# Kernel optimization log

Measured on AMD Instinct MI355X. Metric: run time of the kernel, lower is better.

Reference implementation:

```python
import jax, jax.numpy as jnp
import numpy as np

PATCH = 9
RAD = PATCH // 2  # 4


def _spatial_correlation(a, b):
    """SpatialCorrelationSampler(kernel_size=1, patch_size=9, stride=1,
    padding=0, dilation_patch=1).
    a, b: [B, C, H, W] -> out: [B, 9, 9, H, W]
    out[b, pi, pj, i, j] = sum_c a[b,c,i,j] * b_zeropad[b,c, i+pi-4, j+pj-4]
    Computed one shift at a time (81 small reductions) so we never
    materialize an 81x-unfolded copy of b.
    """
    B, C, H, W = a.shape
    bp = jnp.pad(b, ((0, 0), (0, 0), (RAD, RAD), (RAD, RAD)))
    rows = []
    for di in range(PATCH):
        cols = []
        for dj in range(PATCH):
            # shifted view of b, then channel-dot with a -> [B, H, W]
            cols.append(jnp.sum(a * bp[:, :, di:di + H, dj:dj + W], axis=1))
        rows.append(jnp.stack(cols, axis=1))  # [B, 9, H, W]
    return jnp.stack(rows, axis=1)  # [B, 9, 9, H, W]


def setup_inputs() -> dict:
    key = jax.random.key(0)
    shapes = [(8, 64, 112, 112), (8, 128, 56, 56), (8, 256, 28, 28), (8, 512, 14, 14)]
    keys = jax.random.split(key, 8)
    inp = {}
    for i, s in enumerate(shapes):
        inp[f"rgb{i}"] = jax.random.normal(keys[i], s, dtype=jnp.float32)
        inp[f"depth{i}"] = jax.random.normal(keys[4 + i], s, dtype=jnp.float32)
    return inp


def reference(rgb0, rgb1, rgb2, rgb3, depth0, depth1, depth2, depth3):
    rgbs = [rgb0, rgb1, rgb2, rgb3]
    depths = [depth0, depth1, depth2, depth3]
    corrs = []
    for i in range(4):
        corrs.insert(0, _spatial_correlation(rgbs[i], depths[i]))
    # reversed order: (corr3, corr2, corr1, corr0)
    return tuple(corrs)
```

## Files before the change

kernel.cpp:

```cpp
#include <hip/hip_runtime.h>
#include <hip/hip_bf16.h>

#define THREADS 256

#define OFF3 0
#define OFF2 127008
#define OFF1 635040
#define OFF0 2667168

#define N1 2032128
#define N2 508032
#define N3 127008
#define WS_L1 0
#define WS_L2 (2 * N1)
#define WS_L3 (WS_L2 + 4 * N2)
#define WS_FLOATS (WS_L3 + 16 * N3)
#define WS_BYTES ((size_t)WS_FLOATS * 4)

#define GB_L0 448
#define GB_L1 224
#define GB_L2 224
#define GB_L3 112
#define GB_TOT (GB_L0 + GB_L1 + GB_L2 + GB_L3)

#define SMEM_FLOATS 9728

typedef __attribute__((ext_vector_type(8))) short bf16x8;
typedef __attribute__((ext_vector_type(4))) float f32x4;

__device__ __attribute__((aligned(64))) const float g_zeropage[16] = {};

__global__ void __launch_bounds__(THREADS)
zero_region_kernel(float* __restrict__ p, int n) {
    int i = blockIdx.x * blockDim.x + threadIdx.x;
    int stride = gridDim.x * blockDim.x;
    for (; i < n; i += stride) p[i] = 0.f;
}

__device__ __forceinline__ void gload16(const float* g, float* l) {
    __builtin_amdgcn_global_load_lds(
        (const __attribute__((address_space(1))) void*)g,
        (__attribute__((address_space(3))) void*)l, 16, 0, 0);
}
__device__ __forceinline__ void gload4(const float* g, float* l) {
    __builtin_amdgcn_global_load_lds(
        (const __attribute__((address_space(1))) void*)g,
        (__attribute__((address_space(3))) void*)l, 4, 0, 0);
}

__device__ __forceinline__ short bf16s(float f) {
    __hip_bfloat16 h = __float2bfloat16(f);
    return *reinterpret_cast<short*>(&h);
}

template<int N> __device__ __forceinline__ void wait_vm_lgkm0() {
    static_assert(N >= 0 && N <= 8, "unsupported count");
    if constexpr (N == 0) asm volatile("s_waitcnt vmcnt(0) lgkmcnt(0)" ::: "memory");
    else if constexpr (N == 1) asm volatile("s_waitcnt vmcnt(1) lgkmcnt(0)" ::: "memory");
    else if constexpr (N == 2) asm volatile("s_waitcnt vmcnt(2) lgkmcnt(0)" ::: "memory");
    else if constexpr (N == 3) asm volatile("s_waitcnt vmcnt(3) lgkmcnt(0)" ::: "memory");
    else if constexpr (N == 4) asm volatile("s_waitcnt vmcnt(4) lgkmcnt(0)" ::: "memory");
    else if constexpr (N == 5) asm volatile("s_waitcnt vmcnt(5) lgkmcnt(0)" ::: "memory");
    else if constexpr (N == 6) asm volatile("s_waitcnt vmcnt(6) lgkmcnt(0)" ::: "memory");
    else if constexpr (N == 7) asm volatile("s_waitcnt vmcnt(7) lgkmcnt(0)" ::: "memory");
    else                       asm volatile("s_waitcnt vmcnt(8) lgkmcnt(0)" ::: "memory");
}

template<int C, int H, int W, int TI, int TW, int SJ, int STRIPS, int CHUNKS,
         int CB, int MODE>
__device__ __forceinline__ void corr_level(const float* __restrict__ a,
                                           const float* __restrict__ b,
                                           float* __restrict__ out,
                                           int blk, float* __restrict__ smem)
{
    constexpr int PER_I = 9 * STRIPS;
    constexpr int USED  = TI * PER_I;
    constexpr bool F4   = (W % 4 == 0) && (TW % 4 == 0) && (SJ % 4 == 0);
    constexpr int BWQ0  = (TW + 8 + 3) / 4 + 1;
    constexpr int BWQ   = (BWQ0 % 2 == 0) ? BWQ0 + 1 : BWQ0;
    constexpr int BW_   = F4 ? BWQ * 4 : (((TW + 8 + 1) / 2) * 2);
    constexpr bool F2   = !F4 && (SJ % 2 == 0) && (TW % 2 == 0);
    constexpr int BROWS = TI + 8;
    constexpr int CCH   = C / CHUNKS;
    constexpr int HT    = (H + TI - 1) / TI;
    constexpr int WT    = W / TW;
    constexpr int NOUT  = 8 * 81 * H * W;
    constexpr int HW    = H * W;
    constexpr int BPC   = BROWS * BW_;
    constexpr int APC   = TI * TW;
    constexpr int NG    = CCH / CB;

    constexpr int F4PR = BW_ / 4;
    constexpr int NBF4 = BROWS * F4PR;
    constexpr int TOT4 = CB * NBF4;
    constexpr int K4   = (TOT4 + THREADS - 1) / THREADS;
    constexpr int TOTS = CB * BPC;
    constexpr int KS   = (TOTS + THREADS - 1) / THREADS;
    constexpr int A4PR = TW / 4;
    constexpr int NAF4 = TI * A4PR;
    constexpr int ATOT4 = CB * NAF4;
    constexpr int KA4  = (ATOT4 + THREADS - 1) / THREADS;
    constexpr int ATOTS = CB * APC;
    constexpr int KAS  = (ATOTS + THREADS - 1) / THREADS;

    constexpr int A_OFF = F4 ? (K4 * THREADS * 4) : (KS * THREADS);
    constexpr int BUFSZ = F4 ? ((K4 + KA4) * THREADS * 4) : ((KS + KAS) * THREADS);
    constexpr int KTOT  = F4 ? (K4 + KA4) : (KS + KAS);

    static_assert(USED <= THREADS && SJ * STRIPS == TW && CCH % CB == 0, "geom");
    static_assert(NG >= 2 && 3 * BUFSZ <= SMEM_FLOATS, "pipeline/smem");

    const int ch = blk % CHUNKS;
    int t = blk / CHUNKS;
    const int jt = t % WT; t /= WT;
    const int it = t % HT;
    const int bb = t / HT;
    const int i0 = it * TI;
    const int jb = jt * TW;

    const int tid = threadIdx.x;
    const int ii  = tid / PER_I;
    const int rem = tid - ii * PER_I;
    const int pi  = rem / STRIPS;
    const int s   = rem - pi * STRIPS;
    const int j0  = s * SJ;
    const bool active = (tid < USED) && ((H % TI == 0) || (i0 + ii) < H);

    const int c0 = ch * CCH;
    const float* __restrict__ bp = b + (size_t)(bb * C + c0) * HW;
    const float* __restrict__ ap = a + (size_t)(bb * C + c0) * HW;
    const float* zp = g_zeropage;

    float acc[9][SJ];
    #pragma unroll
    for (int p = 0; p < 9; ++p)
        #pragma unroll
        for (int u = 0; u < SJ; ++u) acc[p][u] = 0.f;

    const int wbase = tid & ~63;

    auto stage = [&](int cg, float* buf) {
        const float* gb = bp + (size_t)(cg * CB) * HW;
        const float* ga = ap + (size_t)(cg * CB) * HW;
        if constexpr (F4) {
            #pragma unroll
            for (int k = 0; k < K4; ++k) {
                const int f = tid + k * THREADS;
                const int cb  = f / NBF4;
                const int f2  = f - cb * NBF4;
                const int row = f2 / F4PR;
                const int c4  = f2 - row * F4PR;
                const int r   = i0 + row - 4;
                const int jj  = jb + (c4 - 1) * 4;
                const bool ok = (f < TOT4) && ((unsigned)r < (unsigned)H)
                                && (jj >= 0) && (jj <= W - 4);
                const float* src = ok ? (gb + cb * HW + r * W + jj) : zp;
                gload16(src, buf + (size_t)(k * THREADS + wbase) * 4);
            }
            #pragma unroll
            for (int k = 0; k < KA4; ++k) {
                const int f = tid + k * THREADS;
                const int cb  = f / NAF4;
                const int f2  = f - cb * NAF4;
                const int row = f2 / A4PR;
                const int c4  = f2 - row * A4PR;
                const bool ok = (f < ATOT4) && ((H % TI == 0) || (i0 + row) < H);
                const float* src = ok ? (ga + cb * HW + (i0 + row) * W + jb + c4 * 4)
                                      : zp;
                gload16(src, buf + A_OFF + (size_t)(k * THREADS + wbase) * 4);
            }
        } else {
            #pragma unroll
            for (int k = 0; k < KS; ++k) {
                const int f = tid + k * THREADS;
                const int cb  = f / BPC;
                const int f2  = f - cb * BPC;
                const int row = f2 / BW_;
                const int col = f2 - row * BW_;
                const int r   = i0 + row - 4;
                const int jj  = jb + col - 4;
                const bool ok = (f < TOTS) && ((unsigned)r < (unsigned)H)
                                && ((unsigned)jj < (unsigned)W);
                const float* src = ok ? (gb + cb * HW + r * W + jj) : zp;
                gload4(src, buf + (k * THREADS + wbase));
            }
            #pragma unroll
            for (int k = 0; k < KAS; ++k) {
                const int f = tid + k * THREADS;
                const int cb  = f / APC;
                const int f2  = f - cb * APC;
                const int row = f2 / TW;
                const int col = f2 - row * TW;
                const bool ok = (f < ATOTS) && ((H % TI == 0) || (i0 + row) < H);
                const float* src = ok ? (ga + cb * HW + (i0 + row) * W + jb + col)
                                      : zp;
                gload4(src, buf + A_OFF + (k * THREADS + wbase));
            }
        }
    };
    auto compute = [&](const float* buf) {
        if (!active) return;
        #pragma unroll
        for (int cb = 0; cb < CB; ++cb) {
            float breg[SJ + 8];
            float areg[SJ];
            const float* bbase = &buf[cb * BPC + (ii + pi) * BW_ + j0];
            const float* abase = &buf[A_OFF + cb * APC + ii * TW + j0];
            if constexpr (F4) {
                #pragma unroll
                for (int k = 0; k < (SJ + 8) / 4; ++k) {
                    float4 v = *reinterpret_cast<const float4*>(&bbase[4 * k]);
                    breg[4*k+0] = v.x; breg[4*k+1] = v.y;
                    breg[4*k+2] = v.z; breg[4*k+3] = v.w;
                }
                #pragma unroll
                for (int u = 0; u < SJ / 4; ++u) {
                    float4 v = *reinterpret_cast<const float4*>(&abase[4 * u]);
                    areg[4*u+0] = v.x; areg[4*u+1] = v.y;
                    areg[4*u+2] = v.z; areg[4*u+3] = v.w;
                }
            } else if constexpr (F2) {
                #pragma unroll
                for (int k = 0; k < (SJ + 8) / 2; ++k) {
                    float2 v = *reinterpret_cast<const float2*>(&bbase[2 * k]);
                    breg[2*k+0] = v.x; breg[2*k+1] = v.y;
                }
                #pragma unroll
                for (int u = 0; u < SJ / 2; ++u) {
                    float2 v = *reinterpret_cast<const float2*>(&abase[2 * u]);
                    areg[2*u+0] = v.x; areg[2*u+1] = v.y;
                }
            } else {
                #pragma unroll
                for (int k = 0; k < SJ + 8; ++k) breg[k] = bbase[k];
                #pragma unroll
                for (int u = 0; u < SJ; ++u) areg[u] = abase[u];
            }
            #pragma unroll
            for (int pj = 0; pj < 9; ++pj)
                #pragma unroll
                for (int u = 0; u < SJ; ++u)
                    acc[pj][u] = fmaf(areg[u], breg[u + pj], acc[pj][u]);
        }
    };

    float* bufA = smem;
    float* bufB = smem + BUFSZ;
    float* bufC = smem + 2 * BUFSZ;

    stage(0, bufA);
    stage(1, bufB);
    for (int cg = 0; cg < NG; ++cg) {
        if (cg < NG - 1) wait_vm_lgkm0<KTOT>();
        else             wait_vm_lgkm0<0>();
        __builtin_amdgcn_s_barrier();
        __builtin_amdgcn_sched_barrier(0);
        if (cg + 2 < NG) stage(cg + 2, bufC);
        compute(bufA);
        float* tp = bufA; bufA = bufB; bufB = bufC; bufC = tp;
    }

    if (active) {
        const int i = i0 + ii;
        float* obase = out;
        if constexpr (MODE == 1) obase = out + (size_t)ch * NOUT;
        #pragma unroll
        for (int pj = 0; pj < 9; ++pj) {
            float* o = obase + ((size_t)((bb * 9 + pi) * 9 + pj) * H + i) * W + jb + j0;
            if constexpr (MODE == 2) {
                #pragma unroll
                for (int u = 0; u < SJ; ++u) atomicAdd(&o[u], acc[pj][u]);
            } else if constexpr (F4) {
                #pragma unroll
                for (int u = 0; u < SJ / 4; ++u) {
                    float4 v;
                    v.x = acc[pj][4*u+0]; v.y = acc[pj][4*u+1];
                    v.z = acc[pj][4*u+2]; v.w = acc[pj][4*u+3];
                    *reinterpret_cast<float4*>(&o[4 * u]) = v;
                }
            } else {
                #pragma unroll
                for (int u = 0; u < SJ; ++u) o[u] = acc[pj][u];
            }
        }
    }
}

__device__ __forceinline__ void corr_l3_mfma(const float* __restrict__ a,
                                             const float* __restrict__ b,
                                             float* __restrict__ out,
                                             int blk, float* __restrict__ smem)
{
    constexpr int C = 512, HW = 196, W = 14;
    const int bb = blk / 14, i = blk % 14;
    const int y0a = ((i - 4) * W) & ~3;
    const int x0a = (i * W) & ~3;
    const int off = i * W - x0a;
    const int tid = threadIdx.x;
    const int lane = tid & 63, wid = tid >> 6;

    float* bl = smem;
    float* al = smem + 32 * 144;
    const float* zp = g_zeropage;
    const float* ab = a + (size_t)bb * C * HW;
    const float* bbase = b + (size_t)bb * C * HW;

    const int nt0 = wid * 2;
    const int ntc = (wid == 3) ? 3 : 2;

    f32x4 accv[3];
    #pragma unroll
    for (int t = 0; t < 3; ++t) accv[t] = (f32x4){0.f, 0.f, 0.f, 0.f};

    const int kgrp = lane >> 4;
    const int mn   = lane & 15;

    for (int ks = 0; ks < 16; ++ks) {
        __syncthreads();
        const float* bp = bbase + (size_t)(ks * 32) * HW;
        #pragma unroll
        for (int it = 0; it < 5; ++it) {
            const int f = tid + it * 256;
            if (f < 1152) {
                const int c = f / 36, q = f - 36 * c;
                const int y = y0a + 4 * q;
                const float* src = (y >= 0 && y <= 192) ? (bp + c * HW + y) : zp;
                gload16(src, smem + (size_t)4 * f);
            }
        }
        if (tid < 160) {
            const int c = tid / 5, q = tid - 5 * c;
            const int x = x0a + 4 * q;
            const float* src = (x <= 192) ? (ab + (size_t)(ks * 32 + c) * HW + x)
                                          : zp;
            gload16(src, smem + (size_t)4 * 1152 + (size_t)4 * tid);
        }
        __syncthreads();

        bf16x8 afr;
        #pragma unroll
        for (int e = 0; e < 8; ++e)
            afr[e] = bf16s(al[(kgrp * 8 + e) * 20 + off + mn]);

        #pragma unroll
        for (int t = 0; t < 3; ++t) {
            if (t < ntc) {
                const int nt = nt0 + t;
                bf16x8 bfr;
                #pragma unroll
                for (int e = 0; e < 8; ++e)
                    bfr[e] = bf16s(bl[(kgrp * 8 + e) * 144 + nt * 16 + mn]);
                accv[t] = __builtin_amdgcn_mfma_f32_16x16x32_bf16(
                    afr, bfr, accv[t], 0, 0, 0);
            }
        }
    }

    const int mrow0 = (lane >> 4) * 4;
    #pragma unroll
    for (int t = 0; t < 3; ++t) {
        if (t < ntc) {
            const int nt = nt0 + t;
            const int y  = y0a + nt * 16 + mn;
            const int ys = y + 56;
            const int yq = ys / 14;
            const int yi = yq - 4;
            const int yj = ys - 14 * yq;
            #pragma unroll
            for (int r = 0; r < 4; ++r) {
                const int m = mrow0 + r;
                const int x = i * 14 + m;
                if (x < 196) {
                    const int xi = x / 14;
                    const int xj = x - 14 * xi;
                    const int pi = yi - xi + 4;
                    const int pj = yj - xj + 4;
                    if ((unsigned)pi < 9u && (unsigned)pj < 9u)
                        out[(size_t)((bb * 9 + pi) * 9 + pj) * HW + x] = accv[t][r];
                }
            }
        }
    }
}

__device__ __forceinline__ void corr_l2_mfma(const float* __restrict__ a,
                                             const float* __restrict__ b,
                                             float* __restrict__ out,
                                             int blk, float* __restrict__ smem)
{
    constexpr int C = 256, HW = 784, W = 28;
    const int bb = blk / 28, i = blk % 28;
    const int x0 = i * 28;
    const int y0 = x0 - 116;
    const int tid = threadIdx.x;
    const int lane = tid & 63, wid = tid >> 6;

    float* bl = smem;
    float* al = smem + 32 * 272;
    const float* zp = g_zeropage;
    const float* ab = a + (size_t)bb * C * HW;
    const float* bbase = b + (size_t)bb * C * HW;

    f32x4 accv[9];
    #pragma unroll
    for (int t = 0; t < 9; ++t) accv[t] = (f32x4){0.f, 0.f, 0.f, 0.f};

    const int kgrp = lane >> 4;
    const int mn   = lane & 15;

    for (int ks = 0; ks < 8; ++ks) {
        __syncthreads();
        const float* bp = bbase + (size_t)(ks * 32) * HW;
        #pragma unroll
        for (int it = 0; it < 9; ++it) {
            const int f = tid + it * 256;
            if (f < 2176) {
                const int c = f / 68, q = f - 68 * c;
                const int y = y0 + 4 * q;
                const float* src = (y >= 0 && y <= HW - 4) ? (bp + c * HW + y) : zp;
                gload16(src, smem + (size_t)4 * f);
            }
        }
        {
            const int c = tid >> 3, q = tid & 7;
            const int x = x0 + 4 * q;
            const float* src = (x <= HW - 4) ? (ab + (size_t)(ks * 32 + c) * HW + x)
                                             : zp;
            gload16(src, smem + (size_t)4 * 2176 + (size_t)4 * tid);
        }
        __syncthreads();

        bf16x8 afr[2];
        #pragma unroll
        for (int mt = 0; mt < 2; ++mt)
            #pragma unroll
            for (int e = 0; e < 8; ++e)
                afr[mt][e] = bf16s(al[(kgrp * 8 + e) * 32 + mt * 16 + mn]);

        #pragma unroll
        for (int t = 0; t < 9; ++t) {
            const int p = wid + 4 * t;
            if (p < 34) {
                const int mt = p & 1, nt = p >> 1;
                bf16x8 bfr;
                #pragma unroll
                for (int e = 0; e < 8; ++e)
                    bfr[e] = bf16s(bl[(kgrp * 8 + e) * 272 + nt * 16 + mn]);
                accv[t] = __builtin_amdgcn_mfma_f32_16x16x32_bf16(
                    afr[mt], bfr, accv[t], 0, 0, 0);
            }
        }
    }

    const int mrow0 = (lane >> 4) * 4;
    #pragma unroll
    for (int t = 0; t < 9; ++t) {
        const int p = wid + 4 * t;
        if (p < 34) {
            const int mt = p & 1, nt = p >> 1;
            const int y  = y0 + nt * 16 + mn;
            const int ys = y + 224;
            const int yq = ys / 28;
            const int yi = yq - 8;
            const int yj = ys - 28 * yq;
            #pragma unroll
            for (int r = 0; r < 4; ++r) {
                const int m = mt * 16 + mrow0 + r;
                const int x = x0 + m;
                if (x < HW) {
                    const int xi = x / 28;
                    const int xj = x - 28 * xi;
                    const int pi = yi - xi + 4;
                    const int pj = yj - xj + 4;
                    if ((unsigned)pi < 9u && (unsigned)pj < 9u)
                        out[(size_t)((bb * 9 + pi) * 9 + pj) * HW + x] = accv[t][r];
                }
            }
        }
    }
}

template<int PMODE>
__global__ void __launch_bounds__(THREADS)
corr_fused(const float* __restrict__ a0, const float* __restrict__ b0,
           const float* __restrict__ a1, const float* __restrict__ b1,
           const float* __restrict__ a2, const float* __restrict__ b2,
           const float* __restrict__ a3, const float* __restrict__ b3,
           float* __restrict__ out, float* __restrict__ ws)
{
    __shared__ float smem[SMEM_FLOATS];
    const int bid = blockIdx.x;
    if (bid < GB_L0) {
        const int blk = (bid % 8) * (GB_L0 / 8) + bid / 8;
        corr_level<64, 112, 112, 4, 56, 8, 7, 1, 2, 0>(
            a0, b0, out + OFF0, blk, smem);
    } else if (bid < GB_L0 + GB_L1) {
        const int r = bid - GB_L0;
        const int blk = (r % 8) * (GB_L1 / 8) + r / 8;
        corr_level<128, 56, 56, 4, 56, 8, 7, 2, 2, PMODE>(
            a1, b1, PMODE == 1 ? ws + WS_L1 : out + OFF1, blk, smem);
    } else if (bid < GB_L0 + GB_L1 + GB_L2) {
        const int r = bid - (GB_L0 + GB_L1);
        const int blk = (r % 8) * (GB_L2 / 8) + r / 8;
        corr_l2_mfma(a2, b2, out + OFF2, blk, smem);
    } else {
        const int r = bid - (GB_L0 + GB_L1 + GB_L2);
        const int blk = (r % 8) * (GB_L3 / 8) + r / 8;
        corr_l3_mfma(a3, b3, out + OFF3, blk, smem);
    }
}

__global__ void __launch_bounds__(THREADS)
reduce_all_kernel(const float* __restrict__ ws, float* __restrict__ out)
{
    const float4* src = (const float4*)(ws + WS_L1);
    float4* dst = (float4*)(out + OFF1);
    const int n4 = N1 / 4;
    for (int i = blockIdx.x * THREADS + threadIdx.x; i < n4;
         i += gridDim.x * THREADS) {
        float4 sv = src[i];
        float4 tv = src[(size_t)n4 + i];
        sv.x += tv.x; sv.y += tv.y; sv.z += tv.z; sv.w += tv.w;
        dst[i] = sv;
    }
}

extern "C" void kernel_launch(void* const* d_in, const int* in_sizes, int n_in,
                              void* d_out, int out_size, void* d_ws, size_t ws_size,
                              hipStream_t stream) {
    const float* a0 = (const float*)d_in[0];
    const float* b0 = (const float*)d_in[1];
    const float* a1 = (const float*)d_in[2];
    const float* b1 = (const float*)d_in[3];
    const float* a2 = (const float*)d_in[4];
    const float* b2 = (const float*)d_in[5];
    const float* a3 = (const float*)d_in[6];
    const float* b3 = (const float*)d_in[7];
    float* out = (float*)d_out;
    float* ws  = (float*)d_ws;

    if (ws_size >= WS_BYTES) {
        hipLaunchKernelGGL((corr_fused<1>), dim3(GB_TOT), dim3(THREADS), 0, stream,
                           a0, b0, a1, b1, a2, b2, a3, b3, out, ws);
        hipLaunchKernelGGL(reduce_all_kernel, dim3(288), dim3(THREADS), 0, stream,
                           ws, out);
    } else {
        hipLaunchKernelGGL(zero_region_kernel, dim3(512), dim3(THREADS), 0, stream,
                           out + OFF1, OFF0 - OFF1);
        hipLaunchKernelGGL((corr_fused<2>), dim3(GB_TOT), dim3(THREADS), 0, stream,
                           a0, b0, a1, b1, a2, b2, a3, b3, out, ws);
    }
}
```

Measured before the change: 60.64 us.

## Replace FP32 FMA correlation for large levels with bf16 MFMA x-tile kernel

```diff
diff --git a/kernel.cpp b/kernel.cpp
--- a/kernel.cpp
+++ b/kernel.cpp
@@ -8,17 +8,8 @@
 #define OFF1 635040
 #define OFF0 2667168
 
-#define N1 2032128
-#define N2 508032
-#define N3 127008
-#define WS_L1 0
-#define WS_L2 (2 * N1)
-#define WS_L3 (WS_L2 + 4 * N2)
-#define WS_FLOATS (WS_L3 + 16 * N3)
-#define WS_BYTES ((size_t)WS_FLOATS * 4)
-
-#define GB_L0 448
-#define GB_L1 224
+#define GB_L0 6272
+#define GB_L1 1792
 #define GB_L2 224
 #define GB_L3 112
 #define GB_TOT (GB_L0 + GB_L1 + GB_L2 + GB_L3)
@@ -29,258 +20,118 @@
 typedef __attribute__((ext_vector_type(4))) float f32x4;
 
 __device__ __attribute__((aligned(64))) const float g_zeropage[16] = {};
-
-__global__ void __launch_bounds__(THREADS)
-zero_region_kernel(float* __restrict__ p, int n) {
-    int i = blockIdx.x * blockDim.x + threadIdx.x;
-    int stride = gridDim.x * blockDim.x;
-    for (; i < n; i += stride) p[i] = 0.f;
-}
 
 __device__ __forceinline__ void gload16(const float* g, float* l) {
     __builtin_amdgcn_global_load_lds(
         (const __attribute__((address_space(1))) void*)g,
         (__attribute__((address_space(3))) void*)l, 16, 0, 0);
 }
-__device__ __forceinline__ void gload4(const float* g, float* l) {
-    __builtin_amdgcn_global_load_lds(
-        (const __attribute__((address_space(1))) void*)g,
-        (__attribute__((address_space(3))) void*)l, 4, 0, 0);
-}
 
 __device__ __forceinline__ short bf16s(float f) {
     __hip_bfloat16 h = __float2bfloat16(f);
     return *reinterpret_cast<short*>(&h);
 }
 
-template<int N> __device__ __forceinline__ void wait_vm_lgkm0() {
-    static_assert(N >= 0 && N <= 8, "unsupported count");
-    if constexpr (N == 0) asm volatile("s_waitcnt vmcnt(0) lgkmcnt(0)" ::: "memory");
-    else if constexpr (N == 1) asm volatile("s_waitcnt vmcnt(1) lgkmcnt(0)" ::: "memory");
-    else if constexpr (N == 2) asm volatile("s_waitcnt vmcnt(2) lgkmcnt(0)" ::: "memory");
-    else if constexpr (N == 3) asm volatile("s_waitcnt vmcnt(3) lgkmcnt(0)" ::: "memory");
-    else if constexpr (N == 4) asm volatile("s_waitcnt vmcnt(4) lgkmcnt(0)" ::: "memory");
-    else if constexpr (N == 5) asm volatile("s_waitcnt vmcnt(5) lgkmcnt(0)" ::: "memory");
-    else if constexpr (N == 6) asm volatile("s_waitcnt vmcnt(6) lgkmcnt(0)" ::: "memory");
-    else if constexpr (N == 7) asm volatile("s_waitcnt vmcnt(7) lgkmcnt(0)" ::: "memory");
-    else                       asm volatile("s_waitcnt vmcnt(8) lgkmcnt(0)" ::: "memory");
-}
-
-template<int C, int H, int W, int TI, int TW, int SJ, int STRIPS, int CHUNKS,
-         int CB, int MODE>
-__device__ __forceinline__ void corr_level(const float* __restrict__ a,
-                                           const float* __restrict__ b,
-                                           float* __restrict__ out,
-                                           int blk, float* __restrict__ smem)
+template<int C, int H, int W, int JT>
+__device__ __forceinline__ void corr_xtile_mfma(const float* __restrict__ a,
+                                                const float* __restrict__ b,
+                                                float* __restrict__ out,
+                                                int blk, float* __restrict__ smem)
 {
-    constexpr int PER_I = 9 * STRIPS;
-    constexpr int USED  = TI * PER_I;
-    constexpr bool F4   = (W % 4 == 0) && (TW % 4 == 0) && (SJ % 4 == 0);
-    constexpr int BWQ0  = (TW + 8 + 3) / 4 + 1;
-    constexpr int BWQ   = (BWQ0 % 2 == 0) ? BWQ0 + 1 : BWQ0;
-    constexpr int BW_   = F4 ? BWQ * 4 : (((TW + 8 + 1) / 2) * 2);
-    constexpr bool F2   = !F4 && (SJ % 2 == 0) && (TW % 2 == 0);
-    constexpr int BROWS = TI + 8;
-    constexpr int CCH   = C / CHUNKS;
-    constexpr int HT    = (H + TI - 1) / TI;
-    constexpr int WT    = W / TW;
-    constexpr int NOUT  = 8 * 81 * H * W;
-    constexpr int HW    = H * W;
-    constexpr int BPC   = BROWS * BW_;
-    constexpr int APC   = TI * TW;
-    constexpr int NG    = CCH / CB;
-
-    constexpr int F4PR = BW_ / 4;
-    constexpr int NBF4 = BROWS * F4PR;
-    constexpr int TOT4 = CB * NBF4;
-    constexpr int K4   = (TOT4 + THREADS - 1) / THREADS;
-    constexpr int TOTS = CB * BPC;
-    constexpr int KS   = (TOTS + THREADS - 1) / THREADS;
-    constexpr int A4PR = TW / 4;
-    constexpr int NAF4 = TI * A4PR;
-    constexpr int ATOT4 = CB * NAF4;
-    constexpr int KA4  = (ATOT4 + THREADS - 1) / THREADS;
-    constexpr int ATOTS = CB * APC;
-    constexpr int KAS  = (ATOTS + THREADS - 1) / THREADS;
-
-    constexpr int A_OFF = F4 ? (K4 * THREADS * 4) : (KS * THREADS);
-    constexpr int BUFSZ = F4 ? ((K4 + KA4) * THREADS * 4) : ((KS + KAS) * THREADS);
-    constexpr int KTOT  = F4 ? (K4 + KA4) : (KS + KAS);
-
-    static_assert(USED <= THREADS && SJ * STRIPS == TW && CCH % CB == 0, "geom");
-    static_assert(NG >= 2 && 3 * BUFSZ <= SMEM_FLOATS, "pipeline/smem");
-
-    const int ch = blk % CHUNKS;
-    int t = blk / CHUNKS;
-    const int jt = t % WT; t /= WT;
-    const int it = t % HT;
-    const int bb = t / HT;
-    const int i0 = it * TI;
-    const int jb = jt * TW;
+    constexpr int HW  = H * W;
+    constexpr int NKS = C / 32;
+    const int bb = blk / (H * JT);
+    const int r2 = blk - bb * (H * JT);
+    const int i  = r2 / JT;
+    const int jt = r2 - i * JT;
+    const int j0 = 16 * jt;
+    const int x0 = i * W + j0;
 
     const int tid = threadIdx.x;
-    const int ii  = tid / PER_I;
-    const int rem = tid - ii * PER_I;
-    const int pi  = rem / STRIPS;
-    const int s   = rem - pi * STRIPS;
-    const int j0  = s * SJ;
-    const bool active = (tid < USED) && ((H % TI == 0) || (i0 + ii) < H);
-
-    const int c0 = ch * CCH;
-    const float* __restrict__ bp = b + (size_t)(bb * C + c0) * HW;
-    const float* __restrict__ ap = a + (size_t)(bb * C + c0) * HW;
+    const int lane = tid & 63, wid = tid >> 6;
+    const int kgrp = lane >> 4, mn = lane & 15;
     const float* zp = g_zeropage;
 
-    float acc[9][SJ];
-    #pragma unroll
-    for (int p = 0; p < 9; ++p)
-        #pragma unroll
-        for (int u = 0; u < SJ; ++u) acc[p][u] = 0.f;
-
-    const int wbase = tid & ~63;
-
-    auto stage = [&](int cg, float* buf) {
-        const float* gb = bp + (size_t)(cg * CB) * HW;
-        const float* ga = ap + (size_t)(cg * CB) * HW;
-        if constexpr (F4) {
-            #pragma unroll
-            for (int k = 0; k < K4; ++k) {
-                const int f = tid + k * THREADS;
-                const int cb  = f / NBF4;
-                const int f2  = f - cb * NBF4;
-                const int row = f2 / F4PR;
-                const int c4  = f2 - row * F4PR;
-                const int r   = i0 + row - 4;
-                const int jj  = jb + (c4 - 1) * 4;
-                const bool ok = (f < TOT4) && ((unsigned)r < (unsigned)H)
-                                && (jj >= 0) && (jj <= W - 4);
-                const float* src = ok ? (gb + cb * HW + r * W + jj) : zp;
-                gload16(src, buf + (size_t)(k * THREADS + wbase) * 4);
-            }
-            #pragma unroll
-            for (int k = 0; k < KA4; ++k) {
-                const int f = tid + k * THREADS;
-                const int cb  = f / NAF4;
-                const int f2  = f - cb * NAF4;
-                const int row = f2 / A4PR;
-                const int c4  = f2 - row * A4PR;
-                const bool ok = (f < ATOT4) && ((H % TI == 0) || (i0 + row) < H);
-                const float* src = ok ? (ga + cb * HW + (i0 + row) * W + jb + c4 * 4)
-                                      : zp;
-                gload16(src, buf + A_OFF + (size_t)(k * THREADS + wbase) * 4);
-            }
-        } else {
-            #pragma unroll
-            for (int k = 0; k < KS; ++k) {
-                const int f = tid + k * THREADS;
-                const int cb  = f / BPC;
-                const int f2  = f - cb * BPC;
-                const int row = f2 / BW_;
-                const int col = f2 - row * BW_;
-                const int r   = i0 + row - 4;
-                const int jj  = jb + col - 4;
-                const bool ok = (f < TOTS) && ((unsigned)r < (unsigned)H)
-                                && ((unsigned)jj < (unsigned)W);
-                const float* src = ok ? (gb + cb * HW + r * W + jj) : zp;
-                gload4(src, buf + (k * THREADS + wbase));
-            }
-            #pragma unroll
-            for (int k = 0; k < KAS; ++k) {
-                const int f = tid + k * THREADS;
-                const int cb  = f / APC;
-                const int f2  = f - cb * APC;
-                const int row = f2 / TW;
-                const int col = f2 - row * TW;
-                const bool ok = (f < ATOTS) && ((H % TI == 0) || (i0 + row) < H);
-                const float* src = ok ? (ga + cb * HW + (i0 + row) * W + jb + col)
-                                      : zp;
-                gload4(src, buf + A_OFF + (k * THREADS + wbase));
-            }
-        }
-    };
-    auto compute = [&](const float* buf) {
-        if (!active) return;
-        #pragma unroll
-        for (int cb = 0; cb < CB; ++cb) {
-            float breg[SJ + 8];
-            float areg[SJ];
-            const float* bbase = &buf[cb * BPC + (ii + pi) * BW_ + j0];
-            const float* abase = &buf[A_OFF + cb * APC + ii * TW + j0];
-            if constexpr (F4) {
+    f32x4 accv[4];
+    #pragma unroll
+    for (int t = 0; t < 4; ++t) accv[t] = (f32x4){0.f, 0.f, 0.f, 0.f};
+
+    for (int ks = 0; ks < NKS; ++ks) {
+        __syncthreads();
+        const float* bp = b + (size_t)(bb * C + ks * 32) * HW;
+        #pragma unroll
+        for (int it = 0; it < 7; ++it) {
+            const int f = tid + it * 256;
+            if (f < 1728) {
+                const int c  = f / 54;
+                const int f2 = f - 54 * c;
+                const int r  = f2 / 6;
+                const int q  = f2 - 6 * r;
+                const int ry = i - 4 + r;
+                const int cy = j0 - 4 + 4 * q;
+                const bool ok = ((unsigned)ry < (unsigned)H)
+                                && (cy >= 0) && (cy <= W - 4);
+                const float* src = ok ? (bp + c * HW + ry * W + cy) : zp;
+                gload16(src, smem + (size_t)4 * f);
+            }
+        }
+        if (tid < 128) {
+            const int c = tid >> 2, q = tid & 3;
+            const int x = x0 + 4 * q;
+            const bool ok = (x <= HW - 4);
+            const float* src = ok ? (a + (size_t)(bb * C + ks * 32 + c) * HW + x)
+                                  : zp;
+            gload16(src, smem + (size_t)(4 * 1728) + (size_t)4 * tid);
+        }
+        __syncthreads();
+
+        bf16x8 afr;
+        #pragma unroll
+        for (int e = 0; e < 8; ++e)
+            afr[e] = bf16s(smem[6912 + (kgrp * 8 + e) * 16 + mn]);
+
+        #pragma unroll
+        for (int t = 0; t < 4; ++t) {
+            const int nt = wid + 4 * t;
+            if (nt < 14) {
+                bf16x8 bfr;
                 #pragma unroll
-                for (int k = 0; k < (SJ + 8) / 4; ++k) {
-                    float4 v = *reinterpret_cast<const float4*>(&bbase[4 * k]);
-                    breg[4*k+0] = v.x; breg[4*k+1] = v.y;
-                    breg[4*k+2] = v.z; breg[4*k+3] = v.w;
+                for (int e = 0; e < 8; ++e) {
+                    const int n = nt * 16 + mn;
+                    bfr[e] = (n < 216)
+                        ? bf16s(smem[(kgrp * 8 + e) * 216 + n]) : (short)0;
                 }
+                accv[t] = __builtin_amdgcn_mfma_f32_16x16x32_bf16(
+                    afr, bfr, accv[t], 0, 0, 0);
+            }
+        }
+    }
+
+    const int mrow0 = (lane >> 4) * 4;
+    #pragma unroll
+    for (int t = 0; t < 4; ++t) {
+        const int nt = wid + 4 * t;
+        if (nt < 14) {
+            const int n = nt * 16 + mn;
+            if (n < 216) {
+                const int ry = n / 24;
+                const int cy = n - 24 * ry;
+                const int yi = i - 4 + ry;
+                const int yj = j0 - 4 + cy;
                 #pragma unroll
-                for (int u = 0; u < SJ / 4; ++u) {
-                    float4 v = *reinterpret_cast<const float4*>(&abase[4 * u]);
-                    areg[4*u+0] = v.x; areg[4*u+1] = v.y;
-                    areg[4*u+2] = v.z; areg[4*u+3] = v.w;
+                for (int r = 0; r < 4; ++r) {
+                    const int m = mrow0 + r;
+                    const int x = x0 + m;
+                    if (x < HW) {
+                        const int xi = x / W;
+                        const int xj = x - W * xi;
+                        const int pi = yi - xi + 4;
+                        const int pj = yj - xj + 4;
+                        if ((unsigned)pi < 9u && (unsigned)pj < 9u)
+                            out[(size_t)((bb * 9 + pi) * 9 + pj) * HW + x]
+                                = accv[t][r];
+                    }
                 }
-            } else if constexpr (F2) {
-                #pragma unroll
-                for (int k = 0; k < (SJ + 8) / 2; ++k) {
-                    float2 v = *reinterpret_cast<const float2*>(&bbase[2 * k]);
-                    breg[2*k+0] = v.x; breg[2*k+1] = v.y;
-                }
-                #pragma unroll
-                for (int u = 0; u < SJ / 2; ++u) {
-                    float2 v = *reinterpret_cast<const float2*>(&abase[2 * u]);
-                    areg[2*u+0] = v.x; areg[2*u+1] = v.y;
-                }
-            } else {
-                #pragma unroll
-                for (int k = 0; k < SJ + 8; ++k) breg[k] = bbase[k];
-                #pragma unroll
-                for (int u = 0; u < SJ; ++u) areg[u] = abase[u];
-            }
-            #pragma unroll
-            for (int pj = 0; pj < 9; ++pj)
-                #pragma unroll
-                for (int u = 0; u < SJ; ++u)
-                    acc[pj][u] = fmaf(areg[u], breg[u + pj], acc[pj][u]);
-        }
-    };
-
-    float* bufA = smem;
-    float* bufB = smem + BUFSZ;
-    float* bufC = smem + 2 * BUFSZ;
-
-    stage(0, bufA);
-    stage(1, bufB);
-    for (int cg = 0; cg < NG; ++cg) {
-        if (cg < NG - 1) wait_vm_lgkm0<KTOT>();
-        else             wait_vm_lgkm0<0>();
-        __builtin_amdgcn_s_barrier();
-        __builtin_amdgcn_sched_barrier(0);
-        if (cg + 2 < NG) stage(cg + 2, bufC);
-        compute(bufA);
-        float* tp = bufA; bufA = bufB; bufB = bufC; bufC = tp;
-    }
-
-    if (active) {
-        const int i = i0 + ii;
-        float* obase = out;
-        if constexpr (MODE == 1) obase = out + (size_t)ch * NOUT;
-        #pragma unroll
-        for (int pj = 0; pj < 9; ++pj) {
-            float* o = obase + ((size_t)((bb * 9 + pi) * 9 + pj) * H + i) * W + jb + j0;
-            if constexpr (MODE == 2) {
-                #pragma unroll
-                for (int u = 0; u < SJ; ++u) atomicAdd(&o[u], acc[pj][u]);
-            } else if constexpr (F4) {
-                #pragma unroll
-                for (int u = 0; u < SJ / 4; ++u) {
-                    float4 v;
-                    v.x = acc[pj][4*u+0]; v.y = acc[pj][4*u+1];
-                    v.z = acc[pj][4*u+2]; v.w = acc[pj][4*u+3];
-                    *reinterpret_cast<float4*>(&o[4 * u]) = v;
-                }
-            } else {
-                #pragma unroll
-                for (int u = 0; u < SJ; ++u) o[u] = acc[pj][u];
             }
         }
     }
@@ -480,25 +331,22 @@
     }
 }
 
-template<int PMODE>
 __global__ void __launch_bounds__(THREADS)
 corr_fused(const float* __restrict__ a0, const float* __restrict__ b0,
            const float* __restrict__ a1, const float* __restrict__ b1,
            const float* __restrict__ a2, const float* __restrict__ b2,
            const float* __restrict__ a3, const float* __restrict__ b3,
-           float* __restrict__ out, float* __restrict__ ws)
+           float* __restrict__ out)
 {
     __shared__ float smem[SMEM_FLOATS];
     const int bid = blockIdx.x;
     if (bid < GB_L0) {
         const int blk = (bid % 8) * (GB_L0 / 8) + bid / 8;
-        corr_level<64, 112, 112, 4, 56, 8, 7, 1, 2, 0>(
-            a0, b0, out + OFF0, blk, smem);
+        corr_xtile_mfma<64, 112, 112, 7>(a0, b0, out + OFF0, blk, smem);
     } else if (bid < GB_L0 + GB_L1) {
         const int r = bid - GB_L0;
         const int blk = (r % 8) * (GB_L1 / 8) + r / 8;
-        corr_level<128, 56, 56, 4, 56, 8, 7, 2, 2, PMODE>(
-            a1, b1, PMODE == 1 ? ws + WS_L1 : out + OFF1, blk, smem);
+        corr_xtile_mfma<128, 56, 56, 4>(a1, b1, out + OFF1, blk, smem);
     } else if (bid < GB_L0 + GB_L1 + GB_L2) {
         const int r = bid - (GB_L0 + GB_L1);
         const int blk = (r % 8) * (GB_L2 / 8) + r / 8;
@@ -507,21 +355,6 @@
         const int r = bid - (GB_L0 + GB_L1 + GB_L2);
         const int blk = (r % 8) * (GB_L3 / 8) + r / 8;
         corr_l3_mfma(a3, b3, out + OFF3, blk, smem);
-    }
-}
-
-__global__ void __launch_bounds__(THREADS)
-reduce_all_kernel(const float* __restrict__ ws, float* __restrict__ out)
-{
-    const float4* src = (const float4*)(ws + WS_L1);
-    float4* dst = (float4*)(out + OFF1);
-    const int n4 = N1 / 4;
-    for (int i = blockIdx.x * THREADS + threadIdx.x; i < n4;
-         i += gridDim.x * THREADS) {
-        float4 sv = src[i];
-        float4 tv = src[(size_t)n4 + i];
-        sv.x += tv.x; sv.y += tv.y; sv.z += tv.z; sv.w += tv.w;
-        dst[i] = sv;
     }
 }
 
@@ -537,17 +370,7 @@
     const float* a3 = (const float*)d_in[6];
     const float* b3 = (const float*)d_in[7];
     float* out = (float*)d_out;
-    float* ws  = (float*)d_ws;
-
-    if (ws_size >= WS_BYTES) {
-        hipLaunchKernelGGL((corr_fused<1>), dim3(GB_TOT), dim3(THREADS), 0, stream,
-                           a0, b0, a1, b1, a2, b2, a3, b3, out, ws);
-        hipLaunchKernelGGL(reduce_all_kernel, dim3(288), dim3(THREADS), 0, stream,
-                           ws, out);
-    } else {
-        hipLaunchKernelGGL(zero_region_kernel, dim3(512), dim3(THREADS), 0, stream,
-                           out + OFF1, OFF0 - OFF1);
-        hipLaunchKernelGGL((corr_fused<2>), dim3(GB_TOT), dim3(THREADS), 0, stream,
-                           a0, b0, a1, b1, a2, b2, a3, b3, out, ws);
-    }
-}
+
+    hipLaunchKernelGGL(corr_fused, dim3(GB_TOT), dim3(THREADS), 0, stream,
+                       a0, b0, a1, b1, a2, b2, a3, b3, out);
+}
```

Measured after the change: 94.98 us. 56.6% more time.
